# Kernel tuning notes

Measured on AMD Instinct MI355X. Metric: run time of the kernel, lower is better.

Reference implementation:

```python
import jax, jax.numpy as jnp
import numpy as np

EMBED_DIM = 1024
NUM_HEADS = 16
HEAD_DIM = EMBED_DIM // NUM_HEADS
SEQ = 2048
BSZ = 4


def setup_inputs() -> dict:
    key = jax.random.key(0)
    k1, k2, k3 = jax.random.split(key, 3)
    x = jax.random.normal(k1, (SEQ, BSZ, EMBED_DIM), dtype=jnp.float32)
    # xavier-uniform-like init for projection weights
    lim_in = float(np.sqrt(6.0 / (EMBED_DIM + 3 * EMBED_DIM)))
    lim_out = float(np.sqrt(6.0 / (EMBED_DIM + EMBED_DIM)))
    W_in = jax.random.uniform(k2, (3 * EMBED_DIM, EMBED_DIM), minval=-lim_in, maxval=lim_in, dtype=jnp.float32)
    b_in = jnp.zeros((3 * EMBED_DIM,), dtype=jnp.float32)
    W_out = jax.random.uniform(k3, (EMBED_DIM, EMBED_DIM), minval=-lim_out, maxval=lim_out, dtype=jnp.float32)
    b_out = jnp.zeros((EMBED_DIM,), dtype=jnp.float32)
    return {"x": x, "W_in": W_in, "b_in": b_in, "W_out": W_out, "b_out": b_out}


def reference(x, W_in, b_in, W_out, b_out):
    # x: [S, B, E] (seq-first, as in the torch module)
    S, B, E = x.shape
    H, D = NUM_HEADS, HEAD_DIM
    qkv = jnp.einsum('sbe,fe->sbf', x, W_in) + b_in          # [S, B, 3E]
    q, k, v = jnp.split(qkv, 3, axis=-1)
    # [S, B, E] -> [B, H, S, D]
    q = q.reshape(S, B, H, D).transpose(1, 2, 0, 3)
    k = k.reshape(S, B, H, D).transpose(1, 2, 0, 3)
    v = v.reshape(S, B, H, D).transpose(1, 2, 0, 3)
    scale = 1.0 / jnp.sqrt(jnp.asarray(D, dtype=x.dtype))
    scores = jnp.einsum('bhsd,bhtd->bhst', q, k) * scale      # [B, H, S, S]
    attn = jax.nn.softmax(scores, axis=-1)                    # dropout p=0.0 -> identity
    out = jnp.einsum('bhst,bhtd->bhsd', attn, v)              # [B, H, S, D]
    out = out.transpose(2, 0, 1, 3).reshape(S, B, E)          # [S, B, E]
    out = jnp.einsum('sbe,fe->sbf', out, W_out) + b_out
    return out, attn
```

## Files before the change

kernel.cpp:

```cpp
#include <hip/hip_runtime.h>
#include <stdint.h>

#define SEQ 2048
#define BSZ 4
#define EMB 1024
#define NH  16
#define HD  64
#define BH  (BSZ*NH)
#define MROWS (SEQ*BSZ)

typedef __attribute__((ext_vector_type(8))) short short8;
typedef __attribute__((ext_vector_type(4))) float f32x4;
typedef __attribute__((ext_vector_type(4))) unsigned short us4;

__device__ __forceinline__ unsigned short f2bf(float f) {
  unsigned u = __float_as_uint(f);
  u += 0x7fffu + ((u >> 16) & 1u);
  return (unsigned short)(u >> 16);
}

#define GLDS(g, l) __builtin_amdgcn_global_load_lds( \
    (const __attribute__((address_space(1))) void*)(g), \
    (__attribute__((address_space(3))) void*)(l), 16, 0, 0)

__global__ void k_cvt(const float* __restrict__ in, unsigned short* __restrict__ out, int n4) {
  int i = blockIdx.x * blockDim.x + threadIdx.x;
  int stride = gridDim.x * blockDim.x;
  for (; i < n4; i += stride) {
    float4 v = reinterpret_cast<const float4*>(in)[i];
    us4 o;
    o[0] = f2bf(v.x); o[1] = f2bf(v.y); o[2] = f2bf(v.z); o[3] = f2bf(v.w);
    reinterpret_cast<us4*>(out)[i] = o;
  }
}

template<int MODE>
__global__ __launch_bounds__(256, 2) void k_gemm_bt(
    const unsigned short* __restrict__ A, const unsigned short* __restrict__ B,
    const float* __restrict__ bias, float* __restrict__ outF,
    unsigned short* __restrict__ qb, unsigned short* __restrict__ kb,
    unsigned short* __restrict__ vb, int M, int N, int K)
{
  __shared__ unsigned short As[128*32];
  __shared__ unsigned short Bs[128*32];
  const int tid  = threadIdx.x;
  const int lane = tid & 63;
  const int wid  = tid >> 6;
  const int wr = wid >> 1, wc = wid & 1;
  const int r0 = blockIdx.y * 128;
  const int c0 = blockIdx.x * 128;
  const int lr = lane & 15;
  const int hi = lane >> 4;

  f32x4 acc[4][4];
  #pragma unroll
  for (int i = 0; i < 4; i++)
    #pragma unroll
    for (int j = 0; j < 4; j++) acc[i][j] = f32x4{0.f,0.f,0.f,0.f};

  const int nk = K >> 5;
  for (int kt = 0; kt < nk; ++kt) {
    #pragma unroll
    for (int j = 0; j < 2; ++j) {
      int e = (wid*2 + j)*512 + lane*8;
      int row = e >> 5, kk = e & 31;
      GLDS(A + (size_t)(r0 + row)*K + kt*32 + kk, &As[(wid*2+j)*512]);
      GLDS(B + (size_t)(c0 + row)*K + kt*32 + kk, &Bs[(wid*2+j)*512]);
    }
    __syncthreads();
    short8 af[4], bf[4];
    #pragma unroll
    for (int i = 0; i < 4; i++) af[i] = *(const short8*)&As[(wr*64 + i*16 + lr)*32 + hi*8];
    #pragma unroll
    for (int j = 0; j < 4; j++) bf[j] = *(const short8*)&Bs[(wc*64 + j*16 + lr)*32 + hi*8];
    #pragma unroll
    for (int i = 0; i < 4; i++)
      #pragma unroll
      for (int j = 0; j < 4; j++)
        acc[i][j] = __builtin_amdgcn_mfma_f32_16x16x32_bf16(af[i], bf[j], acc[i][j], 0, 0, 0);
    __syncthreads();
  }

  #pragma unroll
  for (int i = 0; i < 4; i++) {
    #pragma unroll
    for (int j = 0; j < 4; j++) {
      #pragma unroll
      for (int r = 0; r < 4; r++) {
        int row = r0 + wr*64 + i*16 + hi*4 + r;
        int col = c0 + wc*64 + j*16 + lr;
        float v = acc[i][j][r] + bias[col];
        if (MODE == 0) {
          outF[(size_t)row*N + col] = v;
        } else {
          int s = row >> 2, b = row & 3;
          int which = col >> 10, h = (col >> 6) & 15, d = col & 63;
          unsigned short bvv = f2bf(v);
          unsigned short* dst = (which == 0) ? qb : (which == 1) ? kb : vb;
          dst[((size_t)(b*NH + h)*SEQ + s)*HD + d] = bvv;
        }
      }
    }
  }
}

__global__ void k_transposeV(const unsigned short* __restrict__ V, unsigned short* __restrict__ Vt) {
  __shared__ unsigned short T[64][65];
  const int bh = blockIdx.y;
  const int s0 = blockIdx.x * 64;
  const int t = threadIdx.x;
  const int e = t * 16;
  {
    const int s = e >> 6, d0 = e & 63;
    short8 v0 = *(const short8*)&V[((size_t)bh*SEQ + s0 + s)*HD + d0];
    short8 v1 = *(const short8*)&V[((size_t)bh*SEQ + s0 + s)*HD + d0 + 8];
    #pragma unroll
    for (int q = 0; q < 8; q++) { T[s][d0+q] = (unsigned short)v0[q]; T[s][d0+8+q] = (unsigned short)v1[q]; }
  }
  __syncthreads();
  {
    const int d = e >> 6, sl = e & 63;
    short8 w0, w1;
    #pragma unroll
    for (int q = 0; q < 8; q++) { w0[q] = (short)T[sl+q][d]; w1[q] = (short)T[sl+8+q][d]; }
    *(short8*)&Vt[((size_t)bh*HD + d)*SEQ + s0 + sl]     = w0;
    *(short8*)&Vt[((size_t)bh*HD + d)*SEQ + s0 + sl + 8] = w1;
  }
}

__global__ __launch_bounds__(512, 4) void k_attn5(
    const unsigned short* __restrict__ Q, const unsigned short* __restrict__ Kb,
    const unsigned short* __restrict__ Vt, float* __restrict__ P,
    unsigned short* __restrict__ ctx)
{
  __shared__ unsigned short Ks[3][4096];
  __shared__ unsigned short Vs[3][4096];
  __shared__ float Pf[8][1024];

  const int i   = blockIdx.x;
  const int bh  = i & 63;
  const int rb  = i >> 6;

  const int tid = threadIdx.x;
  const int lane = tid & 63, w = tid >> 6;
  const int lr = lane & 15, hi = lane >> 4;
  const int q0 = rb * 128 + w * 16;
  const size_t qkBase = (size_t)bh * SEQ * HD;
  const size_t vtBase = (size_t)bh * HD * SEQ;

  const int srow = tid >> 3;
  const int scol = ((((tid & 7) * 16) ^ ((srow & 7) << 4)) >> 1);
  const int swz  = (lr & 7) << 4;

  #define STG_K(buf, kt) GLDS(Kb + qkBase + (size_t)((kt)*64 + srow)*HD + scol, \
                              (unsigned short*)Ks[buf] + tid*8)
  #define STG_V(buf, kt) GLDS(Vt + vtBase + (size_t)srow*SEQ + (kt)*64 + scol, \
                              (unsigned short*)Vs[buf] + tid*8)
  #define WAITV(n) asm volatile("s_waitcnt vmcnt(" #n ")" ::: "memory")
  #define BARRIER __builtin_amdgcn_s_barrier(); asm volatile("" ::: "memory")

  short8 bq0 = *(const short8*)&Q[qkBase + (size_t)(q0 + lr)*HD + hi*8];
  short8 bq1 = *(const short8*)&Q[qkBase + (size_t)(q0 + lr)*HD + 32 + hi*8];

  STG_K(0, 0); STG_K(1, 1);
  WAITV(1);
  BARRIER;
  float lsum = 0.f;
  {
    int cur = 0;
    for (int kt = 0; kt < 32; ++kt) {
      const char* kbase = (const char*)Ks[cur];
      #pragma unroll
      for (int ct = 0; ct < 4; ++ct) {
        const int rowb = (ct*16 + lr) * 128;
        short8 ak0 = *(const short8*)(kbase + ((rowb + hi*16) ^ swz));
        short8 ak1 = *(const short8*)(kbase + ((rowb + 64 + hi*16) ^ swz));
        f32x4 z = f32x4{0.f,0.f,0.f,0.f};
        z = __builtin_amdgcn_mfma_f32_16x16x32_bf16(ak0, bq0, z, 0, 0, 0);
        z = __builtin_amdgcn_mfma_f32_16x16x32_bf16(ak1, bq1, z, 0, 0, 0);
        lsum += __expf(z[0]*0.125f) + __expf(z[1]*0.125f)
              + __expf(z[2]*0.125f) + __expf(z[3]*0.125f);
      }
      int bs = cur + 2; if (bs >= 3) bs -= 3;
      if (kt < 30) {
        STG_K(bs, kt + 2);
        WAITV(1);
      } else {
        WAITV(0);
      }
      BARRIER;
      cur = (cur >= 2) ? 0 : cur + 1;
    }
  }
  float lv = lsum;
  lv += __shfl_xor(lv, 16);
  lv += __shfl_xor(lv, 32);
  const float li = 1.0f / lv;

  f32x4 o[4];
  #pragma unroll
  for (int d = 0; d < 4; ++d) o[d] = f32x4{0.f,0.f,0.f,0.f};

  float* pout = P + ((size_t)bh*SEQ + q0)*SEQ;
  char* pfw = (char*)Pf[w];

  STG_K(0, 0); STG_V(0, 0); STG_K(1, 1); STG_V(1, 1);
  WAITV(2);
  BARRIER;
  {
    int cur = 0;
    for (int kt = 0; kt < 32; ++kt) {
      const char* kbase = (const char*)Ks[cur];
      const char* vbase = (const char*)Vs[cur];
      #pragma unroll
      for (int ct = 0; ct < 4; ++ct) {
        const int rowb = (ct*16 + lr) * 128;
        short8 ak0 = *(const short8*)(kbase + ((rowb + hi*16) ^ swz));
        short8 ak1 = *(const short8*)(kbase + ((rowb + 64 + hi*16) ^ swz));
        f32x4 z = f32x4{0.f,0.f,0.f,0.f};
        z = __builtin_amdgcn_mfma_f32_16x16x32_bf16(ak0, bq0, z, 0, 0, 0);
        z = __builtin_amdgcn_mfma_f32_16x16x32_bf16(ak1, bq1, z, 0, 0, 0);
        f32x4 e;
        #pragma unroll
        for (int r = 0; r < 4; r++) e[r] = __expf(z[r]*0.125f) * li;
        *(f32x4*)(pfw + ((((ct*4 + hi) ^ lr) << 4) + lr*256)) = e;
      }
      #pragma unroll
      for (int j = 0; j < 4; ++j) {
        const int row = j*4 + hi;
        f32x4 pv4 = *(const f32x4*)(pfw + (row*256 + ((lr ^ row) << 4)));
        __builtin_nontemporal_store(pv4,
            (f32x4*)&pout[(size_t)row*SEQ + kt*64 + lr*4]);
      }
      #pragma unroll
      for (int s = 0; s < 2; ++s) {
        const int c0 = s*8 + hi*2;
        f32x4 f0 = *(const f32x4*)(pfw + (lr*256 + (((c0    ) ^ lr) << 4)));
        f32x4 f1 = *(const f32x4*)(pfw + (lr*256 + (((c0 + 1) ^ lr) << 4)));
        short8 pa;
        #pragma unroll
        for (int r = 0; r < 4; r++) { pa[r] = (short)f2bf(f0[r]); pa[4+r] = (short)f2bf(f1[r]); }
        #pragma unroll
        for (int dt = 0; dt < 4; ++dt) {
          const int rowb = (dt*16 + lr) * 128;
          short8 vb = *(const short8*)(vbase + ((rowb + s*64 + hi*16) ^ swz));
          o[dt] = __builtin_amdgcn_mfma_f32_16x16x32_bf16(pa, vb, o[dt], 0, 0, 0);
        }
      }
      if (kt < 30) {
        int bs = cur + 2; if (bs >= 3) bs -= 3;
        STG_K(bs, kt + 2); STG_V(bs, kt + 2);
        WAITV(6);
        BARRIER;
      } else if (kt == 30) {
        WAITV(4);
        BARRIER;
      }
      cur = (cur >= 2) ? 0 : cur + 1;
    }
  }

  const int b = bh >> 4, h = bh & 15;
  #pragma unroll
  for (int dt = 0; dt < 4; ++dt)
    #pragma unroll
    for (int r = 0; r < 4; r++) {
      int s = q0 + hi*4 + r;
      ctx[((size_t)s*BSZ + b)*EMB + h*HD + dt*16 + lr] = f2bf(o[dt][r]);
    }
  #undef STG_K
  #undef STG_V
  #undef WAITV
  #undef BARRIER
}

extern "C" void kernel_launch(void* const* d_in, const int* in_sizes, int n_in,
                              void* d_out, int out_size, void* d_ws, size_t ws_size,
                              hipStream_t stream) {
  const float* x     = (const float*)d_in[0];
  const float* W_in  = (const float*)d_in[1];
  const float* b_in  = (const float*)d_in[2];
  const float* W_out = (const float*)d_in[3];
  const float* b_out = (const float*)d_in[4];
  float* out   = (float*)d_out;
  float* attnP = out + (size_t)MROWS*EMB;

  char* ws = (char*)d_ws;
  size_t off = 0;
  auto alloc = [&](size_t bytes) { char* p = ws + off; off += (bytes + 255) & ~255ULL; return p; };
  unsigned short* Xbf    = (unsigned short*)alloc((size_t)MROWS*EMB*2);
  unsigned short* Winbf  = (unsigned short*)alloc((size_t)3*EMB*EMB*2);
  unsigned short* Woutbf = (unsigned short*)alloc((size_t)EMB*EMB*2);
  unsigned short* Qb  = (unsigned short*)alloc((size_t)BH*SEQ*HD*2);
  unsigned short* Kbf = (unsigned short*)alloc((size_t)BH*SEQ*HD*2);
  unsigned short* Vb  = (unsigned short*)alloc((size_t)BH*SEQ*HD*2);
  unsigned short* Vt  = (unsigned short*)alloc((size_t)BH*SEQ*HD*2);
  unsigned short* ctx = Xbf;

  k_cvt<<<2048, 256, 0, stream>>>(x,     Xbf,    MROWS*EMB/4);
  k_cvt<<<1024, 256, 0, stream>>>(W_in,  Winbf,  3*EMB*EMB/4);
  k_cvt<<<512,  256, 0, stream>>>(W_out, Woutbf, EMB*EMB/4);

  k_gemm_bt<1><<<dim3(3*EMB/128, MROWS/128), 256, 0, stream>>>(
      Xbf, Winbf, b_in, nullptr, Qb, Kbf, Vb, MROWS, 3*EMB, EMB);

  k_transposeV<<<dim3(SEQ/64, BH), 256, 0, stream>>>(Vb, Vt);

  k_attn5<<<1024, 512, 0, stream>>>(Qb, Kbf, Vt, attnP, ctx);

  k_gemm_bt<0><<<dim3(EMB/128, MROWS/128), 256, 0, stream>>>(
      ctx, Woutbf, b_out, out, nullptr, nullptr, nullptr, MROWS, EMB, EMB);
}
```

Before: 369.0 us.

## Process two query tiles per attention block and fuse second tile's row-sum pass

Each attention block now handles two 128-row query tiles instead of one, and the grid is halved. The softmax denominator pass for the second tile is computed inside the first tile's probability/PV pass, reusing the same staged K tiles. This cuts total K streaming passes from four to three per pair of tiles. In exchange it raises register pressure and launches only 512 blocks, which may reduce occupancy and latency hiding on a kernel dominated by writing the attention matrix.

```diff
diff --git a/kernel.cpp b/kernel.cpp
--- a/kernel.cpp
+++ b/kernel.cpp
@@ -128,7 +128,7 @@
   }
 }
 
-__global__ __launch_bounds__(512, 4) void k_attn5(
+__global__ __launch_bounds__(512, 4) void k_attn6(
     const unsigned short* __restrict__ Q, const unsigned short* __restrict__ Kb,
     const unsigned short* __restrict__ Vt, float* __restrict__ P,
     unsigned short* __restrict__ ctx)
@@ -144,7 +144,8 @@
   const int tid = threadIdx.x;
   const int lane = tid & 63, w = tid >> 6;
   const int lr = lane & 15, hi = lane >> 4;
-  const int q0 = rb * 128 + w * 16;
+  const int q0A = rb * 256 + w * 16;
+  const int q0B = q0A + 128;
   const size_t qkBase = (size_t)bh * SEQ * HD;
   const size_t vtBase = (size_t)bh * HD * SEQ;
 
@@ -159,13 +160,18 @@
   #define WAITV(n) asm volatile("s_waitcnt vmcnt(" #n ")" ::: "memory")
   #define BARRIER __builtin_amdgcn_s_barrier(); asm volatile("" ::: "memory")
 
-  short8 bq0 = *(const short8*)&Q[qkBase + (size_t)(q0 + lr)*HD + hi*8];
-  short8 bq1 = *(const short8*)&Q[qkBase + (size_t)(q0 + lr)*HD + 32 + hi*8];
+  short8 bqA0 = *(const short8*)&Q[qkBase + (size_t)(q0A + lr)*HD + hi*8];
+  short8 bqA1 = *(const short8*)&Q[qkBase + (size_t)(q0A + lr)*HD + 32 + hi*8];
+  short8 bqB0 = *(const short8*)&Q[qkBase + (size_t)(q0B + lr)*HD + hi*8];
+  short8 bqB1 = *(const short8*)&Q[qkBase + (size_t)(q0B + lr)*HD + 32 + hi*8];
+
+  const int b = bh >> 4, h = bh & 15;
+  char* pfw = (char*)Pf[w];
 
   STG_K(0, 0); STG_K(1, 1);
   WAITV(1);
   BARRIER;
-  float lsum = 0.f;
+  float lsumA = 0.f;
   {
     int cur = 0;
     for (int kt = 0; kt < 32; ++kt) {
@@ -176,10 +182,10 @@
         short8 ak0 = *(const short8*)(kbase + ((rowb + hi*16) ^ swz));
         short8 ak1 = *(const short8*)(kbase + ((rowb + 64 + hi*16) ^ swz));
         f32x4 z = f32x4{0.f,0.f,0.f,0.f};
-        z = __builtin_amdgcn_mfma_f32_16x16x32_bf16(ak0, bq0, z, 0, 0, 0);
-        z = __builtin_amdgcn_mfma_f32_16x16x32_bf16(ak1, bq1, z, 0, 0, 0);
-        lsum += __expf(z[0]*0.125f) + __expf(z[1]*0.125f)
-              + __expf(z[2]*0.125f) + __expf(z[3]*0.125f);
+        z = __builtin_amdgcn_mfma_f32_16x16x32_bf16(ak0, bqA0, z, 0, 0, 0);
+        z = __builtin_amdgcn_mfma_f32_16x16x32_bf16(ak1, bqA1, z, 0, 0, 0);
+        lsumA += __expf(z[0]*0.125f) + __expf(z[1]*0.125f)
+               + __expf(z[2]*0.125f) + __expf(z[3]*0.125f);
       }
       int bs = cur + 2; if (bs >= 3) bs -= 3;
       if (kt < 30) {
@@ -192,17 +198,96 @@
       cur = (cur >= 2) ? 0 : cur + 1;
     }
   }
-  float lv = lsum;
-  lv += __shfl_xor(lv, 16);
-  lv += __shfl_xor(lv, 32);
-  const float li = 1.0f / lv;
-
-  f32x4 o[4];
-  #pragma unroll
-  for (int d = 0; d < 4; ++d) o[d] = f32x4{0.f,0.f,0.f,0.f};
-
-  float* pout = P + ((size_t)bh*SEQ + q0)*SEQ;
-  char* pfw = (char*)Pf[w];
+  float lvA = lsumA;
+  lvA += __shfl_xor(lvA, 16);
+  lvA += __shfl_xor(lvA, 32);
+  const float liA = 1.0f / lvA;
+
+  f32x4 oA[4];
+  #pragma unroll
+  for (int d = 0; d < 4; ++d) oA[d] = f32x4{0.f,0.f,0.f,0.f};
+  float lsumB = 0.f;
+  float* poutA = P + ((size_t)bh*SEQ + q0A)*SEQ;
+
+  STG_K(0, 0); STG_V(0, 0); STG_K(1, 1); STG_V(1, 1);
+  WAITV(2);
+  BARRIER;
+  {
+    int cur = 0;
+    for (int kt = 0; kt < 32; ++kt) {
+      const char* kbase = (const char*)Ks[cur];
+      const char* vbase = (const char*)Vs[cur];
+      #pragma unroll
+      for (int ct = 0; ct < 4; ++ct) {
+        const int rowb = (ct*16 + lr) * 128;
+        short8 ak0 = *(const short8*)(kbase + ((rowb + hi*16) ^ swz));
+        short8 ak1 = *(const short8*)(kbase + ((rowb + 64 + hi*16) ^ swz));
+        f32x4 zA = f32x4{0.f,0.f,0.f,0.f};
+        zA = __builtin_amdgcn_mfma_f32_16x16x32_bf16(ak0, bqA0, zA, 0, 0, 0);
+        zA = __builtin_amdgcn_mfma_f32_16x16x32_bf16(ak1, bqA1, zA, 0, 0, 0);
+        f32x4 zB = f32x4{0.f,0.f,0.f,0.f};
+        zB = __builtin_amdgcn_mfma_f32_16x16x32_bf16(ak0, bqB0, zB, 0, 0, 0);
+        zB = __builtin_amdgcn_mfma_f32_16x16x32_bf16(ak1, bqB1, zB, 0, 0, 0);
+        f32x4 e;
+        #pragma unroll
+        for (int r = 0; r < 4; r++) e[r] = __expf(zA[r]*0.125f) * liA;
+        *(f32x4*)(pfw + ((((ct*4 + hi) ^ lr) << 4) + lr*256)) = e;
+        lsumB += __expf(zB[0]*0.125f) + __expf(zB[1]*0.125f)
+               + __expf(zB[2]*0.125f) + __expf(zB[3]*0.125f);
+      }
+      #pragma unroll
+      for (int j = 0; j < 4; ++j) {
+        const int row = j*4 + hi;
+        f32x4 pv4 = *(const f32x4*)(pfw + (row*256 + ((lr ^ row) << 4)));
+        __builtin_nontemporal_store(pv4,
+            (f32x4*)&poutA[(size_t)row*SEQ + kt*64 + lr*4]);
+      }
+      #pragma unroll
+      for (int s = 0; s < 2; ++s) {
+        const int c0 = s*8 + hi*2;
+        f32x4 f0 = *(const f32x4*)(pfw + (lr*256 + (((c0    ) ^ lr) << 4)));
+        f32x4 f1 = *(const f32x4*)(pfw + (lr*256 + (((c0 + 1) ^ lr) << 4)));
+        short8 pa;
+        #pragma unroll
+        for (int r = 0; r < 4; r++) { pa[r] = (short)f2bf(f0[r]); pa[4+r] = (short)f2bf(f1[r]); }
+        #pragma unroll
+        for (int dt = 0; dt < 4; ++dt) {
+          const int rowb = (dt*16 + lr) * 128;
+          short8 vb = *(const short8*)(vbase + ((rowb + s*64 + hi*16) ^ swz));
+          oA[dt] = __builtin_amdgcn_mfma_f32_16x16x32_bf16(pa, vb, oA[dt], 0, 0, 0);
+        }
+      }
+      if (kt < 30) {
+        int bs = cur + 2; if (bs >= 3) bs -= 3;
+        STG_K(bs, kt + 2); STG_V(bs, kt + 2);
+        WAITV(6);
+        BARRIER;
+      } else if (kt == 30) {
+        WAITV(4);
+        BARRIER;
+      } else {
+        BARRIER;
+      }
+      cur = (cur >= 2) ? 0 : cur + 1;
+    }
+  }
+  float lvB = lsumB;
+  lvB += __shfl_xor(lvB, 16);
+  lvB += __shfl_xor(lvB, 32);
+  const float liB = 1.0f / lvB;
+
+  #pragma unroll
+  for (int dt = 0; dt < 4; ++dt)
+    #pragma unroll
+    for (int r = 0; r < 4; r++) {
+      int s = q0A + hi*4 + r;
+      ctx[((size_t)s*BSZ + b)*EMB + h*HD + dt*16 + lr] = f2bf(oA[dt][r]);
+    }
+
+  f32x4 oB[4];
+  #pragma unroll
+  for (int d = 0; d < 4; ++d) oB[d] = f32x4{0.f,0.f,0.f,0.f};
+  float* poutB = P + ((size_t)bh*SEQ + q0B)*SEQ;
 
   STG_K(0, 0); STG_V(0, 0); STG_K(1, 1); STG_V(1, 1);
   WAITV(2);
@@ -218,11 +303,11 @@
         short8 ak0 = *(const short8*)(kbase + ((rowb + hi*16) ^ swz));
         short8 ak1 = *(const short8*)(kbase + ((rowb + 64 + hi*16) ^ swz));
         f32x4 z = f32x4{0.f,0.f,0.f,0.f};
-        z = __builtin_amdgcn_mfma_f32_16x16x32_bf16(ak0, bq0, z, 0, 0, 0);
-        z = __builtin_amdgcn_mfma_f32_16x16x32_bf16(ak1, bq1, z, 0, 0, 0);
+        z = __builtin_amdgcn_mfma_f32_16x16x32_bf16(ak0, bqB0, z, 0, 0, 0);
+        z = __builtin_amdgcn_mfma_f32_16x16x32_bf16(ak1, bqB1, z, 0, 0, 0);
         f32x4 e;
         #pragma unroll
-        for (int r = 0; r < 4; r++) e[r] = __expf(z[r]*0.125f) * li;
+        for (int r = 0; r < 4; r++) e[r] = __expf(z[r]*0.125f) * liB;
         *(f32x4*)(pfw + ((((ct*4 + hi) ^ lr) << 4) + lr*256)) = e;
       }
       #pragma unroll
@@ -230,7 +315,7 @@
         const int row = j*4 + hi;
         f32x4 pv4 = *(const f32x4*)(pfw + (row*256 + ((lr ^ row) << 4)));
         __builtin_nontemporal_store(pv4,
-            (f32x4*)&pout[(size_t)row*SEQ + kt*64 + lr*4]);
+            (f32x4*)&poutB[(size_t)row*SEQ + kt*64 + lr*4]);
       }
       #pragma unroll
       for (int s = 0; s < 2; ++s) {
@@ -244,7 +329,7 @@
         for (int dt = 0; dt < 4; ++dt) {
           const int rowb = (dt*16 + lr) * 128;
           short8 vb = *(const short8*)(vbase + ((rowb + s*64 + hi*16) ^ swz));
-          o[dt] = __builtin_amdgcn_mfma_f32_16x16x32_bf16(pa, vb, o[dt], 0, 0, 0);
+          oB[dt] = __builtin_amdgcn_mfma_f32_16x16x32_bf16(pa, vb, oB[dt], 0, 0, 0);
         }
       }
       if (kt < 30) {
@@ -260,13 +345,12 @@
     }
   }
 
-  const int b = bh >> 4, h = bh & 15;
   #pragma unroll
   for (int dt = 0; dt < 4; ++dt)
     #pragma unroll
     for (int r = 0; r < 4; r++) {
-      int s = q0 + hi*4 + r;
-      ctx[((size_t)s*BSZ + b)*EMB + h*HD + dt*16 + lr] = f2bf(o[dt][r]);
+      int s = q0B + hi*4 + r;
+      ctx[((size_t)s*BSZ + b)*EMB + h*HD + dt*16 + lr] = f2bf(oB[dt][r]);
     }
   #undef STG_K
   #undef STG_V
@@ -306,7 +390,7 @@
 
   k_transposeV<<<dim3(SEQ/64, BH), 256, 0, stream>>>(Vb, Vt);
 
-  k_attn5<<<1024, 512, 0, stream>>>(Qb, Kbf, Vt, attnP, ctx);
+  k_attn6<<<512, 512, 0, stream>>>(Qb, Kbf, Vt, attnP, ctx);
 
   k_gemm_bt<0><<<dim3(EMB/128, MROWS/128), 256, 0, stream>>>(
       ctx, Woutbf, b_out, out, nullptr, nullptr, nullptr, MROWS, EMB, EMB);
```

New measurement: 385.8 us. +4.6%, slower.

## Shrink attention blocks to 256 threads with double buffering and bf16 P staging

Applied to the files above, without the earlier changes.

The attention kernel now uses 256-thread blocks covering 64 query rows, launched as 2048 blocks. K/V staging drops from triple to double buffering, and the next tile's prefetch is issued before the current tile's compute. The per-wave softmax tile is staged in LDS as bf16 instead of fp32, which cuts LDS use roughly in half so more blocks can fit per CU. The trade-off is that the attention probabilities written to the fp32 output are now rounded to bf16 precision, and the shallower buffering leaves less latency hiding per block.

```diff
diff --git a/kernel.cpp b/kernel.cpp
--- a/kernel.cpp
+++ b/kernel.cpp
@@ -128,14 +128,14 @@
   }
 }
 
-__global__ __launch_bounds__(512, 4) void k_attn5(
+__global__ __launch_bounds__(256, 4) void k_attn7(
     const unsigned short* __restrict__ Q, const unsigned short* __restrict__ Kb,
     const unsigned short* __restrict__ Vt, float* __restrict__ P,
     unsigned short* __restrict__ ctx)
 {
-  __shared__ unsigned short Ks[3][4096];
-  __shared__ unsigned short Vs[3][4096];
-  __shared__ float Pf[8][1024];
+  __shared__ unsigned short Ks[2][4096];
+  __shared__ unsigned short Vs[2][4096];
+  __shared__ unsigned short Pb[4][1024];
 
   const int i   = blockIdx.x;
   const int bh  = i & 63;
@@ -144,7 +144,7 @@
   const int tid = threadIdx.x;
   const int lane = tid & 63, w = tid >> 6;
   const int lr = lane & 15, hi = lane >> 4;
-  const int q0 = rb * 128 + w * 16;
+  const int q0 = rb * 64 + w * 16;
   const size_t qkBase = (size_t)bh * SEQ * HD;
   const size_t vtBase = (size_t)bh * HD * SEQ;
 
@@ -152,44 +152,40 @@
   const int scol = ((((tid & 7) * 16) ^ ((srow & 7) << 4)) >> 1);
   const int swz  = (lr & 7) << 4;
 
-  #define STG_K(buf, kt) GLDS(Kb + qkBase + (size_t)((kt)*64 + srow)*HD + scol, \
-                              (unsigned short*)Ks[buf] + tid*8)
-  #define STG_V(buf, kt) GLDS(Vt + vtBase + (size_t)srow*SEQ + (kt)*64 + scol, \
-                              (unsigned short*)Vs[buf] + tid*8)
+  #define STG_K(buf, kt) do { \
+    GLDS(Kb + qkBase + (size_t)((kt)*64 + srow)*HD + scol,      (unsigned short*)Ks[buf] + tid*8); \
+    GLDS(Kb + qkBase + (size_t)((kt)*64 + 32 + srow)*HD + scol, (unsigned short*)Ks[buf] + 2048 + tid*8); } while(0)
+  #define STG_V(buf, kt) do { \
+    GLDS(Vt + vtBase + (size_t)srow*SEQ + (kt)*64 + scol,        (unsigned short*)Vs[buf] + tid*8); \
+    GLDS(Vt + vtBase + (size_t)(32 + srow)*SEQ + (kt)*64 + scol, (unsigned short*)Vs[buf] + 2048 + tid*8); } while(0)
   #define WAITV(n) asm volatile("s_waitcnt vmcnt(" #n ")" ::: "memory")
   #define BARRIER __builtin_amdgcn_s_barrier(); asm volatile("" ::: "memory")
 
   short8 bq0 = *(const short8*)&Q[qkBase + (size_t)(q0 + lr)*HD + hi*8];
   short8 bq1 = *(const short8*)&Q[qkBase + (size_t)(q0 + lr)*HD + 32 + hi*8];
 
-  STG_K(0, 0); STG_K(1, 1);
-  WAITV(1);
+  STG_K(0, 0);
+  WAITV(0);
   BARRIER;
   float lsum = 0.f;
-  {
-    int cur = 0;
-    for (int kt = 0; kt < 32; ++kt) {
-      const char* kbase = (const char*)Ks[cur];
-      #pragma unroll
-      for (int ct = 0; ct < 4; ++ct) {
-        const int rowb = (ct*16 + lr) * 128;
-        short8 ak0 = *(const short8*)(kbase + ((rowb + hi*16) ^ swz));
-        short8 ak1 = *(const short8*)(kbase + ((rowb + 64 + hi*16) ^ swz));
-        f32x4 z = f32x4{0.f,0.f,0.f,0.f};
-        z = __builtin_amdgcn_mfma_f32_16x16x32_bf16(ak0, bq0, z, 0, 0, 0);
-        z = __builtin_amdgcn_mfma_f32_16x16x32_bf16(ak1, bq1, z, 0, 0, 0);
-        lsum += __expf(z[0]*0.125f) + __expf(z[1]*0.125f)
-              + __expf(z[2]*0.125f) + __expf(z[3]*0.125f);
-      }
-      int bs = cur + 2; if (bs >= 3) bs -= 3;
-      if (kt < 30) {
-        STG_K(bs, kt + 2);
-        WAITV(1);
-      } else {
-        WAITV(0);
-      }
+  for (int kt = 0; kt < 32; ++kt) {
+    const int cur = kt & 1;
+    if (kt < 31) STG_K(cur ^ 1, kt + 1);
+    const char* kbase = (const char*)Ks[cur];
+    #pragma unroll
+    for (int ct = 0; ct < 4; ++ct) {
+      const int rowb = (ct*16 + lr) * 128;
+      short8 ak0 = *(const short8*)(kbase + ((rowb + hi*16) ^ swz));
+      short8 ak1 = *(const short8*)(kbase + ((rowb + 64 + hi*16) ^ swz));
+      f32x4 z = f32x4{0.f,0.f,0.f,0.f};
+      z = __builtin_amdgcn_mfma_f32_16x16x32_bf16(ak0, bq0, z, 0, 0, 0);
+      z = __builtin_amdgcn_mfma_f32_16x16x32_bf16(ak1, bq1, z, 0, 0, 0);
+      lsum += __expf(z[0]*0.125f) + __expf(z[1]*0.125f)
+            + __expf(z[2]*0.125f) + __expf(z[3]*0.125f);
+    }
+    if (kt < 31) {
+      WAITV(0);
       BARRIER;
-      cur = (cur >= 2) ? 0 : cur + 1;
     }
   }
   float lv = lsum;
@@ -202,61 +198,57 @@
   for (int d = 0; d < 4; ++d) o[d] = f32x4{0.f,0.f,0.f,0.f};
 
   float* pout = P + ((size_t)bh*SEQ + q0)*SEQ;
-  char* pfw = (char*)Pf[w];
-
-  STG_K(0, 0); STG_V(0, 0); STG_K(1, 1); STG_V(1, 1);
-  WAITV(2);
+  char* pbw = (char*)Pb[w];
+
+  STG_K(0, 0); STG_V(0, 0);
+  WAITV(0);
   BARRIER;
-  {
-    int cur = 0;
-    for (int kt = 0; kt < 32; ++kt) {
-      const char* kbase = (const char*)Ks[cur];
-      const char* vbase = (const char*)Vs[cur];
-      #pragma unroll
-      for (int ct = 0; ct < 4; ++ct) {
-        const int rowb = (ct*16 + lr) * 128;
-        short8 ak0 = *(const short8*)(kbase + ((rowb + hi*16) ^ swz));
-        short8 ak1 = *(const short8*)(kbase + ((rowb + 64 + hi*16) ^ swz));
-        f32x4 z = f32x4{0.f,0.f,0.f,0.f};
-        z = __builtin_amdgcn_mfma_f32_16x16x32_bf16(ak0, bq0, z, 0, 0, 0);
-        z = __builtin_amdgcn_mfma_f32_16x16x32_bf16(ak1, bq1, z, 0, 0, 0);
-        f32x4 e;
-        #pragma unroll
-        for (int r = 0; r < 4; r++) e[r] = __expf(z[r]*0.125f) * li;
-        *(f32x4*)(pfw + ((((ct*4 + hi) ^ lr) << 4) + lr*256)) = e;
+  for (int kt = 0; kt < 32; ++kt) {
+    const int cur = kt & 1;
+    if (kt < 31) { STG_K(cur ^ 1, kt + 1); STG_V(cur ^ 1, kt + 1); }
+    const char* kbase = (const char*)Ks[cur];
+    const char* vbase = (const char*)Vs[cur];
+    #pragma unroll
+    for (int ct = 0; ct < 4; ++ct) {
+      const int rowb = (ct*16 + lr) * 128;
+      short8 ak0 = *(const short8*)(kbase + ((rowb + hi*16) ^ swz));
+      short8 ak1 = *(const short8*)(kbase + ((rowb + 64 + hi*16) ^ swz));
+      f32x4 z = f32x4{0.f,0.f,0.f,0.f};
+      z = __builtin_amdgcn_mfma_f32_16x16x32_bf16(ak0, bq0, z, 0, 0, 0);
+      z = __builtin_amdgcn_mfma_f32_16x16x32_bf16(ak1, bq1, z, 0, 0, 0);
+      us4 pk;
+      #pragma unroll
+      for (int r = 0; r < 4; r++) pk[r] = f2bf(__expf(z[r]*0.125f) * li);
+      *(us4*)(pbw + lr*128 + (((ct*4 + hi) ^ lr) << 3)) = pk;
+    }
+    #pragma unroll
+    for (int j = 0; j < 4; ++j) {
+      const int row = j*4 + hi;
+      us4 t = *(const us4*)(pbw + row*128 + ((lr ^ row) << 3));
+      f32x4 pv4;
+      #pragma unroll
+      for (int r = 0; r < 4; r++) pv4[r] = __uint_as_float(((unsigned)t[r]) << 16);
+      __builtin_nontemporal_store(pv4,
+          (f32x4*)&pout[(size_t)row*SEQ + kt*64 + lr*4]);
+    }
+    #pragma unroll
+    for (int s = 0; s < 2; ++s) {
+      const int g0 = s*8 + hi*2;
+      us4 a0 = *(const us4*)(pbw + lr*128 + (((g0    ) ^ lr) << 3));
+      us4 a1 = *(const us4*)(pbw + lr*128 + (((g0 + 1) ^ lr) << 3));
+      short8 pa;
+      #pragma unroll
+      for (int r = 0; r < 4; r++) { pa[r] = (short)a0[r]; pa[4+r] = (short)a1[r]; }
+      #pragma unroll
+      for (int dt = 0; dt < 4; ++dt) {
+        const int rowb = (dt*16 + lr) * 128;
+        short8 vb = *(const short8*)(vbase + ((rowb + s*64 + hi*16) ^ swz));
+        o[dt] = __builtin_amdgcn_mfma_f32_16x16x32_bf16(pa, vb, o[dt], 0, 0, 0);
       }
-      #pragma unroll
-      for (int j = 0; j < 4; ++j) {
-        const int row = j*4 + hi;
-        f32x4 pv4 = *(const f32x4*)(pfw + (row*256 + ((lr ^ row) << 4)));
-        __builtin_nontemporal_store(pv4,
-            (f32x4*)&pout[(size_t)row*SEQ + kt*64 + lr*4]);
-      }
-      #pragma unroll
-      for (int s = 0; s < 2; ++s) {
-        const int c0 = s*8 + hi*2;
-        f32x4 f0 = *(const f32x4*)(pfw + (lr*256 + (((c0    ) ^ lr) << 4)));
-        f32x4 f1 = *(const f32x4*)(pfw + (lr*256 + (((c0 + 1) ^ lr) << 4)));
-        short8 pa;
-        #pragma unroll
-        for (int r = 0; r < 4; r++) { pa[r] = (short)f2bf(f0[r]); pa[4+r] = (short)f2bf(f1[r]); }
-        #pragma unroll
-        for (int dt = 0; dt < 4; ++dt) {
-          const int rowb = (dt*16 + lr) * 128;
-          short8 vb = *(const short8*)(vbase + ((rowb + s*64 + hi*16) ^ swz));
-          o[dt] = __builtin_amdgcn_mfma_f32_16x16x32_bf16(pa, vb, o[dt], 0, 0, 0);
-        }
-      }
-      if (kt < 30) {
-        int bs = cur + 2; if (bs >= 3) bs -= 3;
-        STG_K(bs, kt + 2); STG_V(bs, kt + 2);
-        WAITV(6);
-        BARRIER;
-      } else if (kt == 30) {
-        WAITV(4);
-        BARRIER;
-      }
-      cur = (cur >= 2) ? 0 : cur + 1;
+    }
+    if (kt < 31) {
+      WAITV(4);
+      BARRIER;
     }
   }
 
@@ -306,7 +298,7 @@
 
   k_transposeV<<<dim3(SEQ/64, BH), 256, 0, stream>>>(Vb, Vt);
 
-  k_attn5<<<1024, 512, 0, stream>>>(Qb, Kbf, Vt, attnP, ctx);
+  k_attn7<<<2048, 256, 0, stream>>>(Qb, Kbf, Vt, attnP, ctx);
 
   k_gemm_bt<0><<<dim3(EMB/128, MROWS/128), 256, 0, stream>>>(
       ctx, Woutbf, b_out, out, nullptr, nullptr, nullptr, MROWS, EMB, EMB);
```

Result: slower. 407.0 us (+10.3%).

## Process two query groups per attention block and write V transposed from GEMM

Applied to the files above, without the earlier changes.

The attention kernel now handles 256 query rows per block (two 16-row groups per wave), so each staged K/V tile in LDS is reused twice. This halves the grid and the K/V global traffic, at the cost of more registers per thread. The QKV GEMM epilogue writes V directly in transposed layout, which removes the separate transpose kernel and its buffer. Those V stores are now strided across sequence positions, so they may coalesce poorly. The vmcnt wait counts are adjusted to account for the extra outstanding nontemporal stores.

```diff
diff --git a/kernel.cpp b/kernel.cpp
--- a/kernel.cpp
+++ b/kernel.cpp
@@ -96,39 +96,16 @@
           int s = row >> 2, b = row & 3;
           int which = col >> 10, h = (col >> 6) & 15, d = col & 63;
           unsigned short bvv = f2bf(v);
-          unsigned short* dst = (which == 0) ? qb : (which == 1) ? kb : vb;
-          dst[((size_t)(b*NH + h)*SEQ + s)*HD + d] = bvv;
+          if (which == 0)      qb[((size_t)(b*NH + h)*SEQ + s)*HD + d] = bvv;
+          else if (which == 1) kb[((size_t)(b*NH + h)*SEQ + s)*HD + d] = bvv;
+          else                 vb[((size_t)(b*NH + h)*HD + d)*SEQ + s] = bvv;
         }
       }
     }
   }
 }
 
-__global__ void k_transposeV(const unsigned short* __restrict__ V, unsigned short* __restrict__ Vt) {
-  __shared__ unsigned short T[64][65];
-  const int bh = blockIdx.y;
-  const int s0 = blockIdx.x * 64;
-  const int t = threadIdx.x;
-  const int e = t * 16;
-  {
-    const int s = e >> 6, d0 = e & 63;
-    short8 v0 = *(const short8*)&V[((size_t)bh*SEQ + s0 + s)*HD + d0];
-    short8 v1 = *(const short8*)&V[((size_t)bh*SEQ + s0 + s)*HD + d0 + 8];
-    #pragma unroll
-    for (int q = 0; q < 8; q++) { T[s][d0+q] = (unsigned short)v0[q]; T[s][d0+8+q] = (unsigned short)v1[q]; }
-  }
-  __syncthreads();
-  {
-    const int d = e >> 6, sl = e & 63;
-    short8 w0, w1;
-    #pragma unroll
-    for (int q = 0; q < 8; q++) { w0[q] = (short)T[sl+q][d]; w1[q] = (short)T[sl+8+q][d]; }
-    *(short8*)&Vt[((size_t)bh*HD + d)*SEQ + s0 + sl]     = w0;
-    *(short8*)&Vt[((size_t)bh*HD + d)*SEQ + s0 + sl + 8] = w1;
-  }
-}
-
-__global__ __launch_bounds__(512, 4) void k_attn5(
+__global__ __launch_bounds__(512, 4) void k_attn8(
     const unsigned short* __restrict__ Q, const unsigned short* __restrict__ Kb,
     const unsigned short* __restrict__ Vt, float* __restrict__ P,
     unsigned short* __restrict__ ctx)
@@ -144,7 +121,7 @@
   const int tid = threadIdx.x;
   const int lane = tid & 63, w = tid >> 6;
   const int lr = lane & 15, hi = lane >> 4;
-  const int q0 = rb * 128 + w * 16;
+  const int q0g[2] = { rb*256 + w*16, rb*256 + 128 + w*16 };
   const size_t qkBase = (size_t)bh * SEQ * HD;
   const size_t vtBase = (size_t)bh * HD * SEQ;
 
@@ -159,13 +136,17 @@
   #define WAITV(n) asm volatile("s_waitcnt vmcnt(" #n ")" ::: "memory")
   #define BARRIER __builtin_amdgcn_s_barrier(); asm volatile("" ::: "memory")
 
-  short8 bq0 = *(const short8*)&Q[qkBase + (size_t)(q0 + lr)*HD + hi*8];
-  short8 bq1 = *(const short8*)&Q[qkBase + (size_t)(q0 + lr)*HD + 32 + hi*8];
+  short8 bq[2][2];
+  #pragma unroll
+  for (int g = 0; g < 2; ++g) {
+    bq[g][0] = *(const short8*)&Q[qkBase + (size_t)(q0g[g] + lr)*HD + hi*8];
+    bq[g][1] = *(const short8*)&Q[qkBase + (size_t)(q0g[g] + lr)*HD + 32 + hi*8];
+  }
 
   STG_K(0, 0); STG_K(1, 1);
   WAITV(1);
   BARRIER;
-  float lsum = 0.f;
+  float lsum[2] = {0.f, 0.f};
   {
     int cur = 0;
     for (int kt = 0; kt < 32; ++kt) {
@@ -175,11 +156,14 @@
         const int rowb = (ct*16 + lr) * 128;
         short8 ak0 = *(const short8*)(kbase + ((rowb + hi*16) ^ swz));
         short8 ak1 = *(const short8*)(kbase + ((rowb + 64 + hi*16) ^ swz));
-        f32x4 z = f32x4{0.f,0.f,0.f,0.f};
-        z = __builtin_amdgcn_mfma_f32_16x16x32_bf16(ak0, bq0, z, 0, 0, 0);
-        z = __builtin_amdgcn_mfma_f32_16x16x32_bf16(ak1, bq1, z, 0, 0, 0);
-        lsum += __expf(z[0]*0.125f) + __expf(z[1]*0.125f)
-              + __expf(z[2]*0.125f) + __expf(z[3]*0.125f);
+        #pragma unroll
+        for (int g = 0; g < 2; ++g) {
+          f32x4 z = f32x4{0.f,0.f,0.f,0.f};
+          z = __builtin_amdgcn_mfma_f32_16x16x32_bf16(ak0, bq[g][0], z, 0, 0, 0);
+          z = __builtin_amdgcn_mfma_f32_16x16x32_bf16(ak1, bq[g][1], z, 0, 0, 0);
+          lsum[g] += __expf(z[0]*0.125f) + __expf(z[1]*0.125f)
+                   + __expf(z[2]*0.125f) + __expf(z[3]*0.125f);
+        }
       }
       int bs = cur + 2; if (bs >= 3) bs -= 3;
       if (kt < 30) {
@@ -192,16 +176,23 @@
       cur = (cur >= 2) ? 0 : cur + 1;
     }
   }
-  float lv = lsum;
-  lv += __shfl_xor(lv, 16);
-  lv += __shfl_xor(lv, 32);
-  const float li = 1.0f / lv;
-
-  f32x4 o[4];
-  #pragma unroll
-  for (int d = 0; d < 4; ++d) o[d] = f32x4{0.f,0.f,0.f,0.f};
-
-  float* pout = P + ((size_t)bh*SEQ + q0)*SEQ;
+  float li[2];
+  #pragma unroll
+  for (int g = 0; g < 2; ++g) {
+    float lv = lsum[g];
+    lv += __shfl_xor(lv, 16);
+    lv += __shfl_xor(lv, 32);
+    li[g] = 1.0f / lv;
+  }
+
+  f32x4 o[2][4];
+  #pragma unroll
+  for (int g = 0; g < 2; ++g)
+    #pragma unroll
+    for (int d = 0; d < 4; ++d) o[g][d] = f32x4{0.f,0.f,0.f,0.f};
+
+  float* pout[2] = { P + ((size_t)bh*SEQ + q0g[0])*SEQ,
+                     P + ((size_t)bh*SEQ + q0g[1])*SEQ };
   char* pfw = (char*)Pf[w];
 
   STG_K(0, 0); STG_V(0, 0); STG_K(1, 1); STG_V(1, 1);
@@ -213,47 +204,50 @@
       const char* kbase = (const char*)Ks[cur];
       const char* vbase = (const char*)Vs[cur];
       #pragma unroll
-      for (int ct = 0; ct < 4; ++ct) {
-        const int rowb = (ct*16 + lr) * 128;
-        short8 ak0 = *(const short8*)(kbase + ((rowb + hi*16) ^ swz));
-        short8 ak1 = *(const short8*)(kbase + ((rowb + 64 + hi*16) ^ swz));
-        f32x4 z = f32x4{0.f,0.f,0.f,0.f};
-        z = __builtin_amdgcn_mfma_f32_16x16x32_bf16(ak0, bq0, z, 0, 0, 0);
-        z = __builtin_amdgcn_mfma_f32_16x16x32_bf16(ak1, bq1, z, 0, 0, 0);
-        f32x4 e;
+      for (int g = 0; g < 2; ++g) {
         #pragma unroll
-        for (int r = 0; r < 4; r++) e[r] = __expf(z[r]*0.125f) * li;
-        *(f32x4*)(pfw + ((((ct*4 + hi) ^ lr) << 4) + lr*256)) = e;
-      }
-      #pragma unroll
-      for (int j = 0; j < 4; ++j) {
-        const int row = j*4 + hi;
-        f32x4 pv4 = *(const f32x4*)(pfw + (row*256 + ((lr ^ row) << 4)));
-        __builtin_nontemporal_store(pv4,
-            (f32x4*)&pout[(size_t)row*SEQ + kt*64 + lr*4]);
-      }
-      #pragma unroll
-      for (int s = 0; s < 2; ++s) {
-        const int c0 = s*8 + hi*2;
-        f32x4 f0 = *(const f32x4*)(pfw + (lr*256 + (((c0    ) ^ lr) << 4)));
-        f32x4 f1 = *(const f32x4*)(pfw + (lr*256 + (((c0 + 1) ^ lr) << 4)));
-        short8 pa;
+        for (int ct = 0; ct < 4; ++ct) {
+          const int rowb = (ct*16 + lr) * 128;
+          short8 ak0 = *(const short8*)(kbase + ((rowb + hi*16) ^ swz));
+          short8 ak1 = *(const short8*)(kbase + ((rowb + 64 + hi*16) ^ swz));
+          f32x4 z = f32x4{0.f,0.f,0.f,0.f};
+          z = __builtin_amdgcn_mfma_f32_16x16x32_bf16(ak0, bq[g][0], z, 0, 0, 0);
+          z = __builtin_amdgcn_mfma_f32_16x16x32_bf16(ak1, bq[g][1], z, 0, 0, 0);
+          f32x4 e;
+          #pragma unroll
+          for (int r = 0; r < 4; r++) e[r] = __expf(z[r]*0.125f) * li[g];
+          *(f32x4*)(pfw + ((((ct*4 + hi) ^ lr) << 4) + lr*256)) = e;
+        }
         #pragma unroll
-        for (int r = 0; r < 4; r++) { pa[r] = (short)f2bf(f0[r]); pa[4+r] = (short)f2bf(f1[r]); }
+        for (int j = 0; j < 4; ++j) {
+          const int row = j*4 + hi;
+          f32x4 pv4 = *(const f32x4*)(pfw + (row*256 + ((lr ^ row) << 4)));
+          __builtin_nontemporal_store(pv4,
+              (f32x4*)&pout[g][(size_t)row*SEQ + kt*64 + lr*4]);
+        }
         #pragma unroll
-        for (int dt = 0; dt < 4; ++dt) {
-          const int rowb = (dt*16 + lr) * 128;
-          short8 vb = *(const short8*)(vbase + ((rowb + s*64 + hi*16) ^ swz));
-          o[dt] = __builtin_amdgcn_mfma_f32_16x16x32_bf16(pa, vb, o[dt], 0, 0, 0);
+        for (int s = 0; s < 2; ++s) {
+          const int c0 = s*8 + hi*2;
+          f32x4 f0 = *(const f32x4*)(pfw + (lr*256 + (((c0    ) ^ lr) << 4)));
+          f32x4 f1 = *(const f32x4*)(pfw + (lr*256 + (((c0 + 1) ^ lr) << 4)));
+          short8 pa;
+          #pragma unroll
+          for (int r = 0; r < 4; r++) { pa[r] = (short)f2bf(f0[r]); pa[4+r] = (short)f2bf(f1[r]); }
+          #pragma unroll
+          for (int dt = 0; dt < 4; ++dt) {
+            const int rowb = (dt*16 + lr) * 128;
+            short8 vb = *(const short8*)(vbase + ((rowb + s*64 + hi*16) ^ swz));
+            o[g][dt] = __builtin_amdgcn_mfma_f32_16x16x32_bf16(pa, vb, o[g][dt], 0, 0, 0);
+          }
         }
       }
       if (kt < 30) {
         int bs = cur + 2; if (bs >= 3) bs -= 3;
         STG_K(bs, kt + 2); STG_V(bs, kt + 2);
-        WAITV(6);
+        WAITV(10);
         BARRIER;
       } else if (kt == 30) {
-        WAITV(4);
+        WAITV(8);
         BARRIER;
       }
       cur = (cur >= 2) ? 0 : cur + 1;
@@ -262,12 +256,14 @@
 
   const int b = bh >> 4, h = bh & 15;
   #pragma unroll
-  for (int dt = 0; dt < 4; ++dt)
-    #pragma unroll
-    for (int r = 0; r < 4; r++) {
-      int s = q0 + hi*4 + r;
-      ctx[((size_t)s*BSZ + b)*EMB + h*HD + dt*16 + lr] = f2bf(o[dt][r]);
-    }
+  for (int g = 0; g < 2; ++g)
+    #pragma unroll
+    for (int dt = 0; dt < 4; ++dt)
+      #pragma unroll
+      for (int r = 0; r < 4; r++) {
+        int s = q0g[g] + hi*4 + r;
+        ctx[((size_t)s*BSZ + b)*EMB + h*HD + dt*16 + lr] = f2bf(o[g][dt][r]);
+      }
   #undef STG_K
   #undef STG_V
   #undef WAITV
@@ -293,7 +289,6 @@
   unsigned short* Woutbf = (unsigned short*)alloc((size_t)EMB*EMB*2);
   unsigned short* Qb  = (unsigned short*)alloc((size_t)BH*SEQ*HD*2);
   unsigned short* Kbf = (unsigned short*)alloc((size_t)BH*SEQ*HD*2);
-  unsigned short* Vb  = (unsigned short*)alloc((size_t)BH*SEQ*HD*2);
   unsigned short* Vt  = (unsigned short*)alloc((size_t)BH*SEQ*HD*2);
   unsigned short* ctx = Xbf;
 
@@ -302,11 +297,9 @@
   k_cvt<<<512,  256, 0, stream>>>(W_out, Woutbf, EMB*EMB/4);
 
   k_gemm_bt<1><<<dim3(3*EMB/128, MROWS/128), 256, 0, stream>>>(
-      Xbf, Winbf, b_in, nullptr, Qb, Kbf, Vb, MROWS, 3*EMB, EMB);
-
-  k_transposeV<<<dim3(SEQ/64, BH), 256, 0, stream>>>(Vb, Vt);
-
-  k_attn5<<<1024, 512, 0, stream>>>(Qb, Kbf, Vt, attnP, ctx);
+      Xbf, Winbf, b_in, nullptr, Qb, Kbf, Vt, MROWS, 3*EMB, EMB);
+
+  k_attn8<<<512, 512, 0, stream>>>(Qb, Kbf, Vt, attnP, ctx);
 
   k_gemm_bt<0><<<dim3(EMB/128, MROWS/128), 256, 0, stream>>>(
       ctx, Woutbf, b_out, out, nullptr, nullptr, nullptr, MROWS, EMB, EMB);
```

Measured after the change: 421.9 us. 1.14x slower.
